# Performance work log

Measured on AMD Instinct MI355X. Metric: run time of the kernel, lower is better.

The kernel has to match this reference:

```python
import jax, jax.numpy as jnp
import numpy as np

NUM_HEADS = 8

def setup_inputs() -> dict:
    key = jax.random.key(0)
    ks = jax.random.split(key, 11)
    T, B, E = 4096, 4, 512
    CK = 1024  # max_seq_len // compressed
    s = 0.02
    return {
        "query": jax.random.normal(ks[0], (T, B, E), jnp.float32),
        "Wq": jax.random.normal(ks[1], (E, E), jnp.float32) * s,
        "bq": jax.random.normal(ks[2], (E,), jnp.float32) * s,
        "Wk": jax.random.normal(ks[3], (E, E), jnp.float32) * s,
        "bk": jax.random.normal(ks[4], (E,), jnp.float32) * s,
        "Wv": jax.random.normal(ks[5], (E, E), jnp.float32) * s,
        "bv": jax.random.normal(ks[6], (E,), jnp.float32) * s,
        "Wck": jax.random.normal(ks[7], (CK, T), jnp.float32) * s,
        "Wcv": jax.random.normal(ks[8], (CK, T), jnp.float32) * s,
        "Wo": jax.random.normal(ks[9], (E, E), jnp.float32) * s,
        "bo": jax.random.normal(ks[10], (E,), jnp.float32) * s,
    }

def reference(query, Wq, bq, Wk, bk, Wv, bv, Wck, Wcv, Wo, bo):
    # query: [T, B, E] (Time x Batch x Channel)
    T, B, E = query.shape
    H = NUM_HEADS
    hd = E // H
    scaling = hd ** -0.5

    # q projection + scaling
    q = (query @ Wq.T + bq) * scaling                       # [T, B, E]
    # learned sequence compression of K/V inputs: [T,B,E] -> [CK,B,E]
    k_in = jnp.einsum('tbe,ct->cbe', query, Wck[:, :T])
    v_in = jnp.einsum('tbe,ct->cbe', query, Wcv[:, :T])
    k = k_in @ Wk.T + bk                                    # [CK, B, E]
    v = v_in @ Wv.T + bv                                    # [CK, B, E]

    # [L, B, E] -> [B*H, L, hd]
    q = q.reshape(T, B * H, hd).transpose(1, 0, 2)
    k = k.reshape(-1, B * H, hd).transpose(1, 0, 2)
    v = v.reshape(-1, B * H, hd).transpose(1, 0, 2)

    attn = jax.nn.softmax(jnp.einsum('bqd,bkd->bqk', q, k), axis=-1)  # [B*H, T, CK]
    out = jnp.einsum('bqk,bkd->bqd', attn, v)               # [B*H, T, hd]
    out = out.transpose(1, 0, 2).reshape(T, B, E)
    return out @ Wo.T + bo
```

## Files before the change

### kernel.cpp

```cpp
#include <hip/hip_runtime.h>

typedef float f32x4 __attribute__((ext_vector_type(4)));
typedef __bf16 bf16x8 __attribute__((ext_vector_type(8)));
typedef __bf16 bf16x4 __attribute__((ext_vector_type(4)));

#define MFMA16(a, b, c) __builtin_amdgcn_mfma_f32_16x16x32_bf16((a), (b), (c), 0, 0, 0)

template<int F> struct Raw;
template<> struct Raw<0> { bf16x8 v; };
template<> struct Raw<1> { f32x4 a, b; };

template<int F>
__device__ __forceinline__ Raw<F> ldraw(const void* p, size_t idx) {
    Raw<F> r;
    if constexpr (F) {
        const float* q = (const float*)p + idx;
        r.a = *(const f32x4*)q;
        r.b = *(const f32x4*)(q + 4);
    } else {
        r.v = *(const bf16x8*)((const __bf16*)p + idx);
    }
    return r;
}
template<int F>
__device__ __forceinline__ bf16x8 toBf(const Raw<F>& r) {
    if constexpr (F) {
        bf16x8 o;
        o[0] = (__bf16)r.a[0]; o[1] = (__bf16)r.a[1]; o[2] = (__bf16)r.a[2]; o[3] = (__bf16)r.a[3];
        o[4] = (__bf16)r.b[0]; o[5] = (__bf16)r.b[1]; o[6] = (__bf16)r.b[2]; o[7] = (__bf16)r.b[3];
        return o;
    } else {
        return r.v;
    }
}

__global__ __launch_bounds__(256) void cvt(
    const float* __restrict__ a0, const float* __restrict__ a1,
    __bf16* __restrict__ o0, __bf16* __restrict__ o1)
{
    const float* a = blockIdx.y ? a1 : a0;
    __bf16* o = blockIdx.y ? o1 : o0;
    size_t i = ((size_t)blockIdx.x * 256 + threadIdx.x) * 4;
    f32x4 v = *(const f32x4*)&a[i];
    bf16x4 r; r[0]=(__bf16)v[0]; r[1]=(__bf16)v[1]; r[2]=(__bf16)v[2]; r[3]=(__bf16)v[3];
    *(bf16x4*)&o[i] = r;
}

__global__ __launch_bounds__(256) void tq(
    const float* __restrict__ q, __bf16* __restrict__ qT)
{
    __shared__ float Ts[64][65];
    const int t0 = blockIdx.x * 64, n0 = blockIdx.y * 64;
    const int tid = threadIdx.x;
    const int r = tid >> 4, c4 = (tid & 15) * 4;
    for (int p = 0; p < 4; p++) {
        f32x4 v = *(const f32x4*)&q[(size_t)(t0 + r + 16 * p) * 2048 + n0 + c4];
        Ts[r + 16 * p][c4 + 0] = v[0];
        Ts[r + 16 * p][c4 + 1] = v[1];
        Ts[r + 16 * p][c4 + 2] = v[2];
        Ts[r + 16 * p][c4 + 3] = v[3];
    }
    __syncthreads();
    for (int p = 0; p < 4; p++) {
        const int nrow = r + 16 * p;
        bf16x4 o;
        o[0] = (__bf16)Ts[c4 + 0][nrow];
        o[1] = (__bf16)Ts[c4 + 1][nrow];
        o[2] = (__bf16)Ts[c4 + 2][nrow];
        o[3] = (__bf16)Ts[c4 + 3][nrow];
        *(bf16x4*)&qT[(size_t)(n0 + nrow) * 4096 + t0 + c4] = o;
    }
}

__global__ __launch_bounds__(256) void tv(
    const __bf16* __restrict__ vp, __bf16* __restrict__ vpT)
{
    __shared__ __bf16 Ts[64][72];
    const int c0 = blockIdx.x * 64;
    const int bh = blockIdx.y, b = bh >> 3, h = bh & 7;
    const int tid = threadIdx.x;
    const int cr = tid >> 3, a8 = (tid & 7) * 8;
    for (int p = 0; p < 2; p++) {
        bf16x8 v = *(const bf16x8*)&vp[(size_t)(4 * (c0 + cr + 32 * p) + b) * 512 + h * 64 + a8];
        *(bf16x8*)&Ts[cr + 32 * p][a8] = v;
    }
    __syncthreads();
    for (int p = 0; p < 2; p++) {
        const int d = cr + 32 * p;
        bf16x8 o;
        for (int u = 0; u < 8; u++) {
            const int pos = a8 + u;
            const int cc = (pos & 3) * 16 + (pos >> 2);
            o[u] = Ts[cc][d];
        }
        *(bf16x8*)&vpT[((size_t)bh * 64 + d) * 1024 + c0 + a8] = o;
    }
}

template<int BM, int AF, int WF, int CF, int BIAS>
__global__ __launch_bounds__(256) void gemm_nt(
    const void* __restrict__ A0, const void* __restrict__ A1,
    const void* __restrict__ W0, const void* __restrict__ W1,
    const void* __restrict__ b0, const void* __restrict__ b1,
    void* __restrict__ C0, void* __restrict__ C1,
    int M, int N, int K, float scale)
{
    const void* A = blockIdx.z ? A1 : A0;
    const void* W = blockIdx.z ? W1 : W0;
    const void* bias = blockIdx.z ? b1 : b0;
    void* C = blockIdx.z ? C1 : C0;

    __shared__ __attribute__((aligned(16))) __bf16 As[BM][72];
    __shared__ __attribute__((aligned(16))) __bf16 Ws[128][72];

    const int n0 = blockIdx.x * 128;
    const int m0 = blockIdx.y * BM;
    const int tid = threadIdx.x;
    const int lane = tid & 63, wv = tid >> 6;
    const int quad = lane >> 4, l15 = lane & 15;
    constexpr int WR = BM / 2, MI = WR / 16;
    const int wrow = (wv >> 1) * WR, wcol = (wv & 1) * 64;

    const int srow = tid >> 3;
    const int scol = (tid & 7) * 8;
    constexpr int AP = BM / 32;

    Raw<AF> pa[AP];
    Raw<WF> pw[4];
    for (int p = 0; p < AP; p++) pa[p] = ldraw<AF>(A, (size_t)(m0 + srow + 32 * p) * K + scol);
    for (int p = 0; p < 4;  p++) pw[p] = ldraw<WF>(W, (size_t)(n0 + srow + 32 * p) * K + scol);

    f32x4 acc[MI][4];
    for (int i = 0; i < MI; i++)
        for (int j = 0; j < 4; j++)
            acc[i][j] = (f32x4){0.f, 0.f, 0.f, 0.f};

    for (int kt = 0; kt < K; kt += 64) {
        for (int p = 0; p < AP; p++) *(bf16x8*)&As[srow + 32 * p][scol] = toBf<AF>(pa[p]);
        for (int p = 0; p < 4;  p++) *(bf16x8*)&Ws[srow + 32 * p][scol] = toBf<WF>(pw[p]);
        __syncthreads();
        if (kt + 64 < K) {
            for (int p = 0; p < AP; p++)
                pa[p] = ldraw<AF>(A, (size_t)(m0 + srow + 32 * p) * K + kt + 64 + scol);
            for (int p = 0; p < 4;  p++)
                pw[p] = ldraw<WF>(W, (size_t)(n0 + srow + 32 * p) * K + kt + 64 + scol);
        }
        bf16x8 a0[MI], a1[MI], bv0[4], bv1[4];
        for (int i = 0; i < MI; i++) {
            a0[i] = *(bf16x8*)&As[wrow + i * 16 + l15][quad * 8];
            a1[i] = *(bf16x8*)&As[wrow + i * 16 + l15][32 + quad * 8];
        }
        for (int j = 0; j < 4; j++) {
            bv0[j] = *(bf16x8*)&Ws[wcol + j * 16 + l15][quad * 8];
            bv1[j] = *(bf16x8*)&Ws[wcol + j * 16 + l15][32 + quad * 8];
        }
        for (int i = 0; i < MI; i++)
            for (int j = 0; j < 4; j++) {
                acc[i][j] = MFMA16(a0[i], bv0[j], acc[i][j]);
                acc[i][j] = MFMA16(a1[i], bv1[j], acc[i][j]);
            }
        __syncthreads();
    }

    for (int i = 0; i < MI; i++) {
        const int rbase = m0 + wrow + i * 16 + quad * 4;
        for (int j = 0; j < 4; j++) {
            const int col = n0 + wcol + j * 16 + l15;
            float bv = 0.f;
            if constexpr (BIAS) bv = ((const float*)bias)[col];
            for (int r = 0; r < 4; r++) {
                float v = (acc[i][j][r] + bv) * scale;
                size_t off = (size_t)(rbase + r) * N + col;
                if constexpr (CF) ((float*)C)[off] = v;
                else              ((__bf16*)C)[off] = (__bf16)v;
            }
        }
    }
}

__global__ __launch_bounds__(256) void attn_kernel(
    const __bf16* __restrict__ qp,
    const __bf16* __restrict__ kp,
    const __bf16* __restrict__ vpT,
    __bf16* __restrict__ out)
{
    const int BE = 2048, CK = 1024;

    const int bh = blockIdx.x;
    const int qt = blockIdx.y;
    const int b = bh >> 3, h = bh & 7;

    __shared__ __attribute__((aligned(16))) __bf16 QPs[2][128][40];
    __shared__ __attribute__((aligned(16))) __bf16 Ks[2][64][40];
    __shared__ __attribute__((aligned(16))) __bf16 VTs[2][64][40];

    const int tid = threadIdx.x;
    const int lane = tid & 63, wv = tid >> 6;
    const int quad = lane >> 4, l15 = lane & 15;

    const size_t ebase = (size_t)b * 512 + h * 64;

    const int srow = tid >> 3;
    const int a8 = (tid & 7) * 8;
    const int hh = a8 >> 5;
    const int c32 = a8 & 31;

    for (int p = 0; p < 4; p++) {
        bf16x8 v = *(const bf16x8*)&qp[(size_t)(qt * 128 + srow + 32 * p) * BE + ebase + a8];
        *(bf16x8*)&QPs[hh][srow + 32 * p][c32] = v;
    }
    __syncthreads();
    bf16x8 aq[2][2];
    for (int m = 0; m < 2; m++)
        for (int kk = 0; kk < 2; kk++)
            aq[m][kk] = *(bf16x8*)&QPs[kk][wv * 32 + m * 16 + l15][quad * 8];

    bf16x8 pk[2], pv[2];
    for (int p = 0; p < 2; p++) {
        pk[p] = *(const bf16x8*)&kp[(size_t)(srow + 32 * p) * BE + ebase + a8];
        pv[p] = *(const bf16x8*)&vpT[((size_t)bh * 64 + srow + 32 * p) * 1024 + a8];
    }

    f32x4 o[2][4];
    for (int m = 0; m < 2; m++)
        for (int dt = 0; dt < 4; dt++) o[m][dt] = (f32x4){0.f, 0.f, 0.f, 0.f};
    float lrow[2][4] = {{0.f,0.f,0.f,0.f},{0.f,0.f,0.f,0.f}};

    for (int c0 = 0; c0 < CK; c0 += 64) {
        for (int p = 0; p < 2; p++) {
            *(bf16x8*)&Ks[hh][srow + 32 * p][c32]  = pk[p];
            *(bf16x8*)&VTs[hh][srow + 32 * p][c32] = pv[p];
        }
        __syncthreads();
        if (c0 + 64 < CK) {
            const int cn = c0 + 64;
            for (int p = 0; p < 2; p++) {
                pk[p] = *(const bf16x8*)&kp[(size_t)(cn + srow + 32 * p) * BE + ebase + a8];
                pv[p] = *(const bf16x8*)&vpT[((size_t)bh * 64 + srow + 32 * p) * 1024 + cn + a8];
            }
        }

        for (int m = 0; m < 2; m++) {
            f32x4 s[4];
            for (int ct = 0; ct < 4; ct++) {
                bf16x8 bk0 = *(bf16x8*)&Ks[0][ct * 16 + l15][quad * 8];
                bf16x8 bk1 = *(bf16x8*)&Ks[1][ct * 16 + l15][quad * 8];
                f32x4 z = (f32x4){0.f, 0.f, 0.f, 0.f};
                z = MFMA16(aq[m][0], bk0, z);
                z = MFMA16(aq[m][1], bk1, z);
                s[ct] = z;
            }
            for (int r = 0; r < 4; r++) {
                bf16x4 pq;
                for (int ct = 0; ct < 4; ct++) {
                    float pp = __builtin_amdgcn_exp2f(s[ct][r]);
                    lrow[m][r] += pp;
                    pq[ct] = (__bf16)pp;
                }
                *(bf16x4*)&QPs[l15 >> 3][wv * 32 + m * 16 + quad * 4 + r][4 * (l15 & 7)] = pq;
            }
        }

        for (int m = 0; m < 2; m++)
            for (int kk = 0; kk < 2; kk++) {
                bf16x8 ap = *(bf16x8*)&QPs[kk][wv * 32 + m * 16 + l15][quad * 8];
                for (int dt = 0; dt < 4; dt++) {
                    bf16x8 bv = *(bf16x8*)&VTs[kk][dt * 16 + l15][quad * 8];
                    o[m][dt] = MFMA16(ap, bv, o[m][dt]);
                }
            }
        __syncthreads();
    }

    for (int m = 0; m < 2; m++)
        for (int r = 0; r < 4; r++) {
            float l = lrow[m][r];
            l += __shfl_xor(l, 1);
            l += __shfl_xor(l, 2);
            l += __shfl_xor(l, 4);
            l += __shfl_xor(l, 8);
            const float inv = 1.0f / l;
            const int t = qt * 128 + wv * 32 + m * 16 + quad * 4 + r;
            for (int dt = 0; dt < 4; dt++)
                out[(size_t)t * BE + ebase + dt * 16 + l15] = (__bf16)(o[m][dt][r] * inv);
        }
}

extern "C" void kernel_launch(void* const* d_in, const int* in_sizes, int n_in,
                              void* d_out, int out_size, void* d_ws, size_t ws_size,
                              hipStream_t stream)
{
    const float* query = (const float*)d_in[0];
    const void* Wq = d_in[1];  const void* bq = d_in[2];
    const void* Wk = d_in[3];  const void* bk = d_in[4];
    const void* Wv = d_in[5];  const void* bv = d_in[6];
    const float* Wck = (const float*)d_in[7];
    const float* Wcv = (const float*)d_in[8];
    const void* Wo = d_in[9];  const void* bo = d_in[10];

    const size_t MiB = 1u << 20;

    __bf16* qT    = (__bf16*)d_ws;
    __bf16* kin   = (__bf16*)((char*)d_ws + 16 * MiB);
    __bf16* vin   = (__bf16*)((char*)d_ws + 20 * MiB);
    __bf16* ao    = (__bf16*)d_ws;

    __bf16* qp    = (__bf16*)d_out;
    __bf16* Wckbf = (__bf16*)((char*)d_out + 16 * MiB);
    __bf16* Wcvbf = (__bf16*)((char*)d_out + 24 * MiB);
    __bf16* kpb   = (__bf16*)((char*)d_out + 16 * MiB);
    __bf16* vp    = (__bf16*)((char*)d_out + 20 * MiB);
    __bf16* vpT   = (__bf16*)((char*)d_out + 24 * MiB);

    cvt<<<dim3(4096, 2), 256, 0, stream>>>(Wck, Wcv, Wckbf, Wcvbf);
    tq<<<dim3(64, 32), 256, 0, stream>>>(query, qT);

    gemm_nt<128, 1, 1, 0, 1><<<dim3(4, 128, 1), 256, 0, stream>>>(
        query, query, Wq, Wq, bq, bq, qp, qp, 16384, 512, 512,
        0.125f * 1.44269504088896f);

    gemm_nt<64, 0, 0, 0, 0><<<dim3(16, 16, 2), 256, 0, stream>>>(
        Wckbf, Wcvbf, qT, qT, nullptr, nullptr, kin, vin, 1024, 2048, 4096, 1.0f);

    gemm_nt<64, 0, 1, 0, 1><<<dim3(4, 64, 2), 256, 0, stream>>>(
        kin, vin, Wk, Wv, bk, bv, kpb, vp, 4096, 512, 512, 1.0f);

    tv<<<dim3(16, 32), 256, 0, stream>>>(vp, vpT);

    attn_kernel<<<dim3(32, 32), 256, 0, stream>>>(qp, kpb, vpT, ao);

    gemm_nt<128, 0, 1, 1, 1><<<dim3(4, 128, 1), 256, 0, stream>>>(
        ao, ao, Wo, Wo, bo, bo, d_out, d_out, 16384, 512, 512, 1.0f);
}
```

Baseline: 297.5 us.

## Double-buffer GEMM LDS tiles with direct global-to-LDS loads and XOR swizzle

Restructures the gemm_nt main loop around two LDS buffers so the next K-tile is staged while the current one is computed, which removes one barrier per iteration. For bf16 operands it uses global_load_lds to copy straight from global memory into LDS, skipping the register round trip. It replaces the padded 72-column layout with an XOR-swizzled 64-column layout to avoid bank conflicts. This doubles LDS use per block, which may lower occupancy. The single barrier per iteration must still order the asynchronous LDS writes against the reads, which is a correctness risk.

```diff
diff --git a/kernel.cpp b/kernel.cpp
--- a/kernel.cpp
+++ b/kernel.cpp
@@ -5,6 +5,12 @@
 typedef __bf16 bf16x4 __attribute__((ext_vector_type(4)));
 
 #define MFMA16(a, b, c) __builtin_amdgcn_mfma_f32_16x16x32_bf16((a), (b), (c), 0, 0, 0)
+
+__device__ __forceinline__ void gl16(const void* g, void* l) {
+    __builtin_amdgcn_global_load_lds(
+        (const __attribute__((address_space(1))) void*)g,
+        (__attribute__((address_space(3))) void*)l, 16, 0, 0);
+}
 
 template<int F> struct Raw;
 template<> struct Raw<0> { bf16x8 v; };
@@ -110,8 +116,8 @@
     const void* bias = blockIdx.z ? b1 : b0;
     void* C = blockIdx.z ? C1 : C0;
 
-    __shared__ __attribute__((aligned(16))) __bf16 As[BM][72];
-    __shared__ __attribute__((aligned(16))) __bf16 Ws[128][72];
+    __shared__ __attribute__((aligned(16))) __bf16 As[2][BM][64];
+    __shared__ __attribute__((aligned(16))) __bf16 Ws[2][128][64];
 
     const int n0 = blockIdx.x * 128;
     const int m0 = blockIdx.y * BM;
@@ -121,38 +127,81 @@
     constexpr int WR = BM / 2, MI = WR / 16;
     const int wrow = (wv >> 1) * WR, wcol = (wv & 1) * 64;
 
+    const int lrow = lane >> 3;
+    const int csrc = ((lane & 7) ^ lrow) * 8;
+
     const int srow = tid >> 3;
-    const int scol = (tid & 7) * 8;
+    const int sj = tid & 7;
+    const int swc = (sj ^ (srow & 7)) * 8;
+
     constexpr int AP = BM / 32;
-
     Raw<AF> pa[AP];
     Raw<WF> pw[4];
-    for (int p = 0; p < AP; p++) pa[p] = ldraw<AF>(A, (size_t)(m0 + srow + 32 * p) * K + scol);
-    for (int p = 0; p < 4;  p++) pw[p] = ldraw<WF>(W, (size_t)(n0 + srow + 32 * p) * K + scol);
+
+    auto stageA = [&](int buf, int kt) {
+        if constexpr (AF == 0) {
+            for (int p = 0; p < AP; p++)
+                gl16((const __bf16*)A + (size_t)(m0 + wv * 8 + p * 32 + lrow) * K + kt + csrc,
+                     &As[buf][wv * 8 + p * 32][0]);
+        } else {
+            (void)kt;
+            for (int p = 0; p < AP; p++)
+                *(bf16x8*)&As[buf][srow + 32 * p][swc] = toBf<AF>(pa[p]);
+        }
+    };
+    auto stageW = [&](int buf, int kt) {
+        if constexpr (WF == 0) {
+            for (int p = 0; p < 4; p++)
+                gl16((const __bf16*)W + (size_t)(n0 + wv * 8 + p * 32 + lrow) * K + kt + csrc,
+                     &Ws[buf][wv * 8 + p * 32][0]);
+        } else {
+            (void)kt;
+            for (int p = 0; p < 4; p++)
+                *(bf16x8*)&Ws[buf][srow + 32 * p][swc] = toBf<WF>(pw[p]);
+        }
+    };
+    auto loadA = [&](int kt) {
+        if constexpr (AF == 1)
+            for (int p = 0; p < AP; p++)
+                pa[p] = ldraw<AF>(A, (size_t)(m0 + srow + 32 * p) * K + kt + sj * 8);
+    };
+    auto loadW = [&](int kt) {
+        if constexpr (WF == 1)
+            for (int p = 0; p < 4; p++)
+                pw[p] = ldraw<WF>(W, (size_t)(n0 + srow + 32 * p) * K + kt + sj * 8);
+    };
 
     f32x4 acc[MI][4];
     for (int i = 0; i < MI; i++)
         for (int j = 0; j < 4; j++)
             acc[i][j] = (f32x4){0.f, 0.f, 0.f, 0.f};
 
-    for (int kt = 0; kt < K; kt += 64) {
-        for (int p = 0; p < AP; p++) *(bf16x8*)&As[srow + 32 * p][scol] = toBf<AF>(pa[p]);
-        for (int p = 0; p < 4;  p++) *(bf16x8*)&Ws[srow + 32 * p][scol] = toBf<WF>(pw[p]);
-        __syncthreads();
-        if (kt + 64 < K) {
-            for (int p = 0; p < AP; p++)
-                pa[p] = ldraw<AF>(A, (size_t)(m0 + srow + 32 * p) * K + kt + 64 + scol);
-            for (int p = 0; p < 4;  p++)
-                pw[p] = ldraw<WF>(W, (size_t)(n0 + srow + 32 * p) * K + kt + 64 + scol);
+    loadA(0);
+    loadW(0);
+    stageA(0, 0);
+    stageW(0, 0);
+    loadA(64);
+    loadW(64);
+    __syncthreads();
+
+    const int NT = K >> 6;
+    for (int t = 0; t < NT; ++t) {
+        const int cur = t & 1;
+        if (t + 1 < NT) {
+            stageA(cur ^ 1, (t + 1) * 64);
+            stageW(cur ^ 1, (t + 1) * 64);
+            if (t + 2 < NT) { loadA((t + 2) * 64); loadW((t + 2) * 64); }
         }
         bf16x8 a0[MI], a1[MI], bv0[4], bv1[4];
         for (int i = 0; i < MI; i++) {
-            a0[i] = *(bf16x8*)&As[wrow + i * 16 + l15][quad * 8];
-            a1[i] = *(bf16x8*)&As[wrow + i * 16 + l15][32 + quad * 8];
+            const int r = wrow + i * 16 + l15;
+            a0[i] = *(const bf16x8*)&As[cur][r][(quad ^ (r & 7)) * 8];
+            a1[i] = *(const bf16x8*)&As[cur][r][((4 + quad) ^ (r & 7)) * 8];
         }
         for (int j = 0; j < 4; j++) {
-            bv0[j] = *(bf16x8*)&Ws[wcol + j * 16 + l15][quad * 8];
-            bv1[j] = *(bf16x8*)&Ws[wcol + j * 16 + l15][32 + quad * 8];
+            const int r = wcol + j * 16 + l15;
+            bv0[j] = *(const bf16x8*)&Ws[cur][r][(quad ^ (r & 7)) * 8];
+            bv1[j] = *(const bf16x8*)&Ws[cur][r][((4 + quad) ^ (r & 7)) * 8];
         }
         for (int i = 0; i < MI; i++)
             for (int j = 0; j < 4; j++) {
@@ -166,10 +215,10 @@
         const int rbase = m0 + wrow + i * 16 + quad * 4;
         for (int j = 0; j < 4; j++) {
             const int col = n0 + wcol + j * 16 + l15;
-            float bv = 0.f;
-            if constexpr (BIAS) bv = ((const float*)bias)[col];
+            float bvv = 0.f;
+            if constexpr (BIAS) bvv = ((const float*)bias)[col];
             for (int r = 0; r < 4; r++) {
-                float v = (acc[i][j][r] + bv) * scale;
+                float v = (acc[i][j][r] + bvv) * scale;
                 size_t off = (size_t)(rbase + r) * N + col;
                 if constexpr (CF) ((float*)C)[off] = v;
                 else              ((__bf16*)C)[off] = (__bf16)v;
@@ -224,7 +273,7 @@
     f32x4 o[2][4];
     for (int m = 0; m < 2; m++)
         for (int dt = 0; dt < 4; dt++) o[m][dt] = (f32x4){0.f, 0.f, 0.f, 0.f};
-    float lrow[2][4] = {{0.f,0.f,0.f,0.f},{0.f,0.f,0.f,0.f}};
+    float lrowv[2][4] = {{0.f,0.f,0.f,0.f},{0.f,0.f,0.f,0.f}};
 
     for (int c0 = 0; c0 < CK; c0 += 64) {
         for (int p = 0; p < 2; p++) {
@@ -254,7 +303,7 @@
                 bf16x4 pq;
                 for (int ct = 0; ct < 4; ct++) {
                     float pp = __builtin_amdgcn_exp2f(s[ct][r]);
-                    lrow[m][r] += pp;
+                    lrowv[m][r] += pp;
                     pq[ct] = (__bf16)pp;
                 }
                 *(bf16x4*)&QPs[l15 >> 3][wv * 32 + m * 16 + quad * 4 + r][4 * (l15 & 7)] = pq;
@@ -274,7 +323,7 @@
 
     for (int m = 0; m < 2; m++)
         for (int r = 0; r < 4; r++) {
-            float l = lrow[m][r];
+            float l = lrowv[m][r];
             l += __shfl_xor(l, 1);
             l += __shfl_xor(l, 2);
             l += __shfl_xor(l, 4);
```

New measurement: 293.6 us. No clear change (-1.3%).
